# Optimization experiments

Measured on AMD Instinct MI355X. Metric: run time of the kernel, lower is better.

Reference implementation:

```python
import jax, jax.numpy as jnp
import numpy as np


def setup_inputs() -> dict:
    key = jax.random.key(0)
    k1, k2, k3, k4 = jax.random.split(key, 4)
    B, IN_DIM, OUT_DIM = 2048, 4096, 4096
    inputs = jax.random.normal(k1, (B, IN_DIM), dtype=jnp.float32)
    # integer weight code: each element of the implicit (in_dim,out_dim) weight
    # matrix is an index into the per-row `mean` vector of length in_dim
    indices = jax.random.randint(k2, (IN_DIM, OUT_DIM), 0, IN_DIM, dtype=jnp.int32)
    mean = jax.random.normal(k3, (IN_DIM,), dtype=jnp.float32)
    bias = jax.random.normal(k4, (OUT_DIM,), dtype=jnp.float32)
    return {"inputs": inputs, "indices": indices, "mean": mean, "bias": bias}


def reference(inputs, indices, mean, bias):
    # 'unsort' op: decode weight W[i,j] = mean[indices[i,j]], then x @ W
    W = mean[indices]                      # (in_dim, out_dim) gather-decode
    out = jnp.einsum("bi,io->bo", inputs, W)  # (batch, out_dim)
    return out + bias                      # channels_last bias add
```

## Files before the change

kernel.cpp:

```cpp
#include <hip/hip_runtime.h>
#include <hip/hip_bf16.h>


#define M_DIM 2048
#define K_DIM 4096
#define N_DIM 4096

typedef __attribute__((ext_vector_type(8))) short short8v;
typedef __attribute__((ext_vector_type(4))) float f32x4;

__device__ __forceinline__ unsigned short f2bf(float x) {
    unsigned u = __builtin_bit_cast(unsigned, x);
    u += 0x7fffu + ((u >> 16) & 1u);
    return (unsigned short)(u >> 16);
}

__device__ __forceinline__ void gload_lds16(const void* g, void* l) {
    __builtin_amdgcn_global_load_lds(
        (const __attribute__((address_space(1))) void*)(uintptr_t)g,
        (__attribute__((address_space(3))) void*)(uintptr_t)l, 16, 0, 0);
}

__global__ void convert_a_kernel(const float* __restrict__ A,
                                 unsigned short* __restrict__ Abf) {
    int i = blockIdx.x * blockDim.x + threadIdx.x;
    const float4 v = ((const float4*)A)[i];
    ushort4 o;
    o.x = f2bf(v.x); o.y = f2bf(v.y); o.z = f2bf(v.z); o.w = f2bf(v.w);
    ((ushort4*)Abf)[i] = o;
}

__global__ void decode_transpose_kernel(const int* __restrict__ idx,
                                        const float* __restrict__ mean,
                                        unsigned short* __restrict__ Wt) {
    __shared__ float smean[K_DIM];
    __shared__ unsigned short tile[64][65];
    const int t = threadIdx.x;
    for (int i = t; i < K_DIM; i += 256) smean[i] = mean[i];
    __syncthreads();

    const int k0 = blockIdx.y * 64;
    const int n0 = blockIdx.x * 64;
    const int rb = t >> 4;
    const int cb = (t & 15) * 4;

    #pragma unroll
    for (int i = 0; i < 4; ++i) {
        const int r = rb + i * 16;
        const int4 v = *(const int4*)&idx[(size_t)(k0 + r) * N_DIM + n0 + cb];
        tile[cb + 0][r] = f2bf(smean[v.x]);
        tile[cb + 1][r] = f2bf(smean[v.y]);
        tile[cb + 2][r] = f2bf(smean[v.z]);
        tile[cb + 3][r] = f2bf(smean[v.w]);
    }
    __syncthreads();

    #pragma unroll
    for (int i = 0; i < 4; ++i) {
        const int r = rb + i * 16;
        ushort4 o;
        o.x = tile[r][cb + 0];
        o.y = tile[r][cb + 1];
        o.z = tile[r][cb + 2];
        o.w = tile[r][cb + 3];
        *(ushort4*)&Wt[(size_t)(n0 + r) * K_DIM + k0 + cb] = o;
    }
}

__global__ void gemm_kernel(const unsigned short* __restrict__ Abf,
                            const unsigned short* __restrict__ Wt,
                            const float* __restrict__ bias,
                            float* __restrict__ C) {
    __shared__ unsigned short sA[128 * 32];
    __shared__ unsigned short sB[128 * 32];

    const int tid  = threadIdx.x;
    const int lane = tid & 63;
    const int w    = tid >> 6;
    const int wm   = w >> 1, wn = w & 1;
    const int m0   = blockIdx.y * 128;
    const int n0   = blockIdx.x * 128;

    f32x4 acc[4][4] = {};

    const int r0   = tid >> 2;
    const int sub0 = (tid & 3) * 16;

    const int lr = lane & 15;
    const int kq = lane >> 4;

    for (int k0 = 0; k0 < K_DIM; k0 += 32) {
        const char* gA0 = (const char*)(Abf + (size_t)(m0 + r0) * K_DIM + k0) + sub0;
        const char* gA1 = (const char*)(Abf + (size_t)(m0 + 64 + r0) * K_DIM + k0) + sub0;
        const char* gB0 = (const char*)(Wt  + (size_t)(n0 + r0) * K_DIM + k0) + sub0;
        const char* gB1 = (const char*)(Wt  + (size_t)(n0 + 64 + r0) * K_DIM + k0) + sub0;
        gload_lds16(gA0, (char*)sA + tid * 16);
        gload_lds16(gA1, (char*)sA + 4096 + tid * 16);
        gload_lds16(gB0, (char*)sB + tid * 16);
        gload_lds16(gB1, (char*)sB + 4096 + tid * 16);
        __syncthreads();

        short8v a[4], b[4];
        #pragma unroll
        for (int i = 0; i < 4; ++i) {
            a[i] = *(const short8v*)&sA[(wm * 64 + i * 16 + lr) * 32 + kq * 8];
            b[i] = *(const short8v*)&sB[(wn * 64 + i * 16 + lr) * 32 + kq * 8];
        }
        #pragma unroll
        for (int i = 0; i < 4; ++i)
            #pragma unroll
            for (int j = 0; j < 4; ++j)
                acc[i][j] = __builtin_amdgcn_mfma_f32_16x16x32_bf16(a[i], b[j], acc[i][j], 0, 0, 0);
        __syncthreads();
    }

    #pragma unroll
    for (int j = 0; j < 4; ++j) {
        const int n = n0 + wn * 64 + j * 16 + lr;
        const float bv = bias[n];
        #pragma unroll
        for (int i = 0; i < 4; ++i) {
            const int mb = m0 + wm * 64 + i * 16 + kq * 4;
            #pragma unroll
            for (int q = 0; q < 4; ++q)
                C[(size_t)(mb + q) * N_DIM + n] = acc[i][j][q] + bv;
        }
    }
}

extern "C" void kernel_launch(void* const* d_in, const int* in_sizes, int n_in,
                              void* d_out, int out_size, void* d_ws, size_t ws_size,
                              hipStream_t stream) {
    const float* inputs  = (const float*)d_in[0];
    const int*   indices = (const int*)  d_in[1];
    const float* mean    = (const float*)d_in[2];
    const float* bias    = (const float*)d_in[3];
    float* out = (float*)d_out;

    unsigned short* Abf = (unsigned short*)d_ws;
    unsigned short* Wt  = (unsigned short*)((char*)d_ws + (size_t)M_DIM * K_DIM * 2);

    convert_a_kernel<<<(M_DIM * K_DIM / 4) / 256, 256, 0, stream>>>(inputs, Abf);
    decode_transpose_kernel<<<dim3(N_DIM / 64, K_DIM / 64), 256, 0, stream>>>(indices, mean, Wt);
    gemm_kernel<<<dim3(N_DIM / 128, M_DIM / 128), 256, 0, stream>>>(Abf, Wt, bias, out);
}
```

Before: 228.2 us.

## Rewrite GEMM with triple-buffered LDS pipeline, larger tiles and swizzle

```diff
diff --git a/kernel.cpp b/kernel.cpp
--- a/kernel.cpp
+++ b/kernel.cpp
@@ -5,6 +5,14 @@
 #define M_DIM 2048
 #define K_DIM 4096
 #define N_DIM 4096
+
+#define BM 128
+#define BN 256
+#define BK 64
+#define NT (K_DIM / BK)
+#define LDSA_BYTES (BM * BK * 2)
+#define LDSB_BYTES (BN * BK * 2)
+#define LDS_TILE   (LDSA_BYTES + LDSB_BYTES)
 
 typedef __attribute__((ext_vector_type(8))) short short8v;
 typedef __attribute__((ext_vector_type(4))) float f32x4;
@@ -67,52 +75,132 @@
     }
 }
 
-__global__ void gemm_kernel(const unsigned short* __restrict__ Abf,
-                            const unsigned short* __restrict__ Wt,
-                            const float* __restrict__ bias,
-                            float* __restrict__ C) {
-    __shared__ unsigned short sA[128 * 32];
-    __shared__ unsigned short sB[128 * 32];
+
+#define VM6 asm volatile("s_waitcnt vmcnt(6)" ::: "memory")
+#define VM0 asm volatile("s_waitcnt vmcnt(0)" ::: "memory")
+#define NOPST ((void)0)
+
+#define STG_FIRST(kst) do {                          \
+    gload_lds16(srcA0 + (kst), pb2 + ldsA0);         \
+    gload_lds16(srcA1 + (kst), pb2 + ldsA1);         \
+    gload_lds16(srcB0 + (kst), pb2 + ldsB0);         \
+} while (0)
+
+#define STG_SECOND(kst) do {                         \
+    gload_lds16(srcB1 + (kst), pb2 + ldsB1);         \
+    gload_lds16(srcB2 + (kst), pb2 + ldsB2);         \
+    gload_lds16(srcB3 + (kst), pb2 + ldsB3);         \
+} while (0)
+
+#define PHASE(kk, STAGES, ENDW) do {                                          \
+    const int sc = ((((kk) * 4) + kq) ^ (lr & 7)) * 16;                       \
+    short8v a0 = *(const short8v*)(pb0 + rA0 + sc);                           \
+    short8v a1 = *(const short8v*)(pb0 + rA1 + sc);                           \
+    short8v a2 = *(const short8v*)(pb0 + rA2 + sc);                           \
+    short8v a3 = *(const short8v*)(pb0 + rA3 + sc);                           \
+    short8v b0 = *(const short8v*)(pb0 + rB0 + sc);                           \
+    short8v b1 = *(const short8v*)(pb0 + rB1 + sc);                           \
+    short8v b2 = *(const short8v*)(pb0 + rB2 + sc);                           \
+    short8v b3 = *(const short8v*)(pb0 + rB3 + sc);                           \
+    STAGES;                                                                   \
+    __builtin_amdgcn_s_barrier();                                             \
+    __builtin_amdgcn_s_setprio(1);                                            \
+    acc[0][0] = __builtin_amdgcn_mfma_f32_16x16x32_bf16(a0, b0, acc[0][0], 0, 0, 0); \
+    acc[0][1] = __builtin_amdgcn_mfma_f32_16x16x32_bf16(a0, b1, acc[0][1], 0, 0, 0); \
+    acc[0][2] = __builtin_amdgcn_mfma_f32_16x16x32_bf16(a0, b2, acc[0][2], 0, 0, 0); \
+    acc[0][3] = __builtin_amdgcn_mfma_f32_16x16x32_bf16(a0, b3, acc[0][3], 0, 0, 0); \
+    acc[1][0] = __builtin_amdgcn_mfma_f32_16x16x32_bf16(a1, b0, acc[1][0], 0, 0, 0); \
+    acc[1][1] = __builtin_amdgcn_mfma_f32_16x16x32_bf16(a1, b1, acc[1][1], 0, 0, 0); \
+    acc[1][2] = __builtin_amdgcn_mfma_f32_16x16x32_bf16(a1, b2, acc[1][2], 0, 0, 0); \
+    acc[1][3] = __builtin_amdgcn_mfma_f32_16x16x32_bf16(a1, b3, acc[1][3], 0, 0, 0); \
+    acc[2][0] = __builtin_amdgcn_mfma_f32_16x16x32_bf16(a2, b0, acc[2][0], 0, 0, 0); \
+    acc[2][1] = __builtin_amdgcn_mfma_f32_16x16x32_bf16(a2, b1, acc[2][1], 0, 0, 0); \
+    acc[2][2] = __builtin_amdgcn_mfma_f32_16x16x32_bf16(a2, b2, acc[2][2], 0, 0, 0); \
+    acc[2][3] = __builtin_amdgcn_mfma_f32_16x16x32_bf16(a2, b3, acc[2][3], 0, 0, 0); \
+    acc[3][0] = __builtin_amdgcn_mfma_f32_16x16x32_bf16(a3, b0, acc[3][0], 0, 0, 0); \
+    acc[3][1] = __builtin_amdgcn_mfma_f32_16x16x32_bf16(a3, b1, acc[3][1], 0, 0, 0); \
+    acc[3][2] = __builtin_amdgcn_mfma_f32_16x16x32_bf16(a3, b2, acc[3][2], 0, 0, 0); \
+    acc[3][3] = __builtin_amdgcn_mfma_f32_16x16x32_bf16(a3, b3, acc[3][3], 0, 0, 0); \
+    __builtin_amdgcn_s_setprio(0);                                            \
+    ENDW;                                                                     \
+    __builtin_amdgcn_s_barrier();                                             \
+    __builtin_amdgcn_sched_barrier(0);                                        \
+} while (0)
+
+__global__ __launch_bounds__(512, 2) void gemm_kernel(
+        const unsigned short* __restrict__ Abf,
+        const unsigned short* __restrict__ Wt,
+        const float* __restrict__ bias,
+        float* __restrict__ C) {
+    __shared__ __align__(128) char lds[3 * LDS_TILE];
 
     const int tid  = threadIdx.x;
     const int lane = tid & 63;
     const int w    = tid >> 6;
-    const int wm   = w >> 1, wn = w & 1;
-    const int m0   = blockIdx.y * 128;
-    const int n0   = blockIdx.x * 128;
+    const int wm   = w >> 2;
+    const int wn   = w & 3;
+    const int lr   = lane & 15;
+    const int kq   = lane >> 4;
+
+    const int bid = blockIdx.x;
+    const int wg  = (bid & 7) * 32 + (bid >> 3);
+    const int m0  = (wg >> 4) * BM;
+    const int n0  = (wg & 15) * BN;
+
+    const int pA0 = tid,        pA1 = 512 + tid;
+    const int pB0 = tid,        pB1 = 512 + tid;
+    const int pB2 = 1024 + tid, pB3 = 1536 + tid;
+    const unsigned short* srcA0 = Abf + (size_t)(m0 + (pA0 >> 3)) * K_DIM + 8 * ((pA0 & 7) ^ ((pA0 >> 3) & 7));
+    const unsigned short* srcA1 = Abf + (size_t)(m0 + (pA1 >> 3)) * K_DIM + 8 * ((pA1 & 7) ^ ((pA1 >> 3) & 7));
+    const unsigned short* srcB0 = Wt  + (size_t)(n0 + (pB0 >> 3)) * K_DIM + 8 * ((pB0 & 7) ^ ((pB0 >> 3) & 7));
+    const unsigned short* srcB1 = Wt  + (size_t)(n0 + (pB1 >> 3)) * K_DIM + 8 * ((pB1 & 7) ^ ((pB1 >> 3) & 7));
+    const unsigned short* srcB2 = Wt  + (size_t)(n0 + (pB2 >> 3)) * K_DIM + 8 * ((pB2 & 7) ^ ((pB2 >> 3) & 7));
+    const unsigned short* srcB3 = Wt  + (size_t)(n0 + (pB3 >> 3)) * K_DIM + 8 * ((pB3 & 7) ^ ((pB3 >> 3) & 7));
+    const int ldsA0 = pA0 * 16, ldsA1 = pA1 * 16;
+    const int ldsB0 = LDSA_BYTES + pB0 * 16, ldsB1 = LDSA_BYTES + pB1 * 16;
+    const int ldsB2 = LDSA_BYTES + pB2 * 16, ldsB3 = LDSA_BYTES + pB3 * 16;
+
+    const int rA0 = (wm * 64 +  0 + lr) * 128;
+    const int rA1 = (wm * 64 + 16 + lr) * 128;
+    const int rA2 = (wm * 64 + 32 + lr) * 128;
+    const int rA3 = (wm * 64 + 48 + lr) * 128;
+    const int rB0 = LDSA_BYTES + (wn * 64 +  0 + lr) * 128;
+    const int rB1 = LDSA_BYTES + (wn * 64 + 16 + lr) * 128;
+    const int rB2 = LDSA_BYTES + (wn * 64 + 32 + lr) * 128;
+    const int rB3 = LDSA_BYTES + (wn * 64 + 48 + lr) * 128;
+
+    char* pb0 = (char*)lds;
+    char* pb1 = (char*)lds + LDS_TILE;
+    char* pb2 = (char*)lds + 2 * LDS_TILE;
 
     f32x4 acc[4][4] = {};
 
-    const int r0   = tid >> 2;
-    const int sub0 = (tid & 3) * 16;
-
-    const int lr = lane & 15;
-    const int kq = lane >> 4;
-
-    for (int k0 = 0; k0 < K_DIM; k0 += 32) {
-        const char* gA0 = (const char*)(Abf + (size_t)(m0 + r0) * K_DIM + k0) + sub0;
-        const char* gA1 = (const char*)(Abf + (size_t)(m0 + 64 + r0) * K_DIM + k0) + sub0;
-        const char* gB0 = (const char*)(Wt  + (size_t)(n0 + r0) * K_DIM + k0) + sub0;
-        const char* gB1 = (const char*)(Wt  + (size_t)(n0 + 64 + r0) * K_DIM + k0) + sub0;
-        gload_lds16(gA0, (char*)sA + tid * 16);
-        gload_lds16(gA1, (char*)sA + 4096 + tid * 16);
-        gload_lds16(gB0, (char*)sB + tid * 16);
-        gload_lds16(gB1, (char*)sB + 4096 + tid * 16);
-        __syncthreads();
-
-        short8v a[4], b[4];
-        #pragma unroll
-        for (int i = 0; i < 4; ++i) {
-            a[i] = *(const short8v*)&sA[(wm * 64 + i * 16 + lr) * 32 + kq * 8];
-            b[i] = *(const short8v*)&sB[(wn * 64 + i * 16 + lr) * 32 + kq * 8];
-        }
-        #pragma unroll
-        for (int i = 0; i < 4; ++i)
-            #pragma unroll
-            for (int j = 0; j < 4; ++j)
-                acc[i][j] = __builtin_amdgcn_mfma_f32_16x16x32_bf16(a[i], b[j], acc[i][j], 0, 0, 0);
-        __syncthreads();
-    }
+    gload_lds16(srcA0 + 0, pb0 + ldsA0);
+    gload_lds16(srcA1 + 0, pb0 + ldsA1);
+    gload_lds16(srcB0 + 0, pb0 + ldsB0);
+    gload_lds16(srcB1 + 0, pb0 + ldsB1);
+    gload_lds16(srcB2 + 0, pb0 + ldsB2);
+    gload_lds16(srcB3 + 0, pb0 + ldsB3);
+    gload_lds16(srcA0 + BK, pb1 + ldsA0);
+    gload_lds16(srcA1 + BK, pb1 + ldsA1);
+    gload_lds16(srcB0 + BK, pb1 + ldsB0);
+    gload_lds16(srcB1 + BK, pb1 + ldsB1);
+    gload_lds16(srcB2 + BK, pb1 + ldsB2);
+    gload_lds16(srcB3 + BK, pb1 + ldsB3);
+    VM6;
+    __builtin_amdgcn_s_barrier();
+
+    for (int t = 0; t < NT - 2; ++t) {
+        const int kst = (t + 2) * BK;
+        PHASE(0, STG_FIRST(kst), NOPST);
+        PHASE(1, STG_SECOND(kst), VM6);
+        char* tmp = pb0; pb0 = pb1; pb1 = pb2; pb2 = tmp;
+    }
+    PHASE(0, NOPST, NOPST);
+    PHASE(1, NOPST, VM0);
+    pb0 = pb1;
+    PHASE(0, NOPST, NOPST);
+    PHASE(1, NOPST, NOPST);
 
     #pragma unroll
     for (int j = 0; j < 4; ++j) {
@@ -142,5 +230,5 @@
 
     convert_a_kernel<<<(M_DIM * K_DIM / 4) / 256, 256, 0, stream>>>(inputs, Abf);
     decode_transpose_kernel<<<dim3(N_DIM / 64, K_DIM / 64), 256, 0, stream>>>(indices, mean, Wt);
-    gemm_kernel<<<dim3(N_DIM / 128, M_DIM / 128), 256, 0, stream>>>(Abf, Wt, bias, out);
-}
+    gemm_kernel<<<256, 512, 0, stream>>>(Abf, Wt, bias, out);
+}
```

Result: faster. 209.8 us (-8.1%).

## Rewrite GEMM with 4-stage LDS pipeline, 128x256 tiles, swizzle and XCD remap

Applied to the files above, without the earlier changes.

```diff
diff --git a/kernel.cpp b/kernel.cpp
--- a/kernel.cpp
+++ b/kernel.cpp
@@ -5,6 +5,14 @@
 #define M_DIM 2048
 #define K_DIM 4096
 #define N_DIM 4096
+
+#define BM 128
+#define BN 256
+#define BK 32
+#define NT (K_DIM / BK)
+#define TILE_A (BM * BK * 2)
+#define TILE_B (BN * BK * 2)
+#define TILE   (TILE_A + TILE_B)
 
 typedef __attribute__((ext_vector_type(8))) short short8v;
 typedef __attribute__((ext_vector_type(4))) float f32x4;
@@ -67,60 +75,150 @@
     }
 }
 
-__global__ void gemm_kernel(const unsigned short* __restrict__ Abf,
-                            const unsigned short* __restrict__ Wt,
-                            const float* __restrict__ bias,
-                            float* __restrict__ C) {
-    __shared__ unsigned short sA[128 * 32];
-    __shared__ unsigned short sB[128 * 32];
+
+#define VM6  asm volatile("s_waitcnt vmcnt(6)" ::: "memory")
+#define VM0  asm volatile("s_waitcnt vmcnt(0)" ::: "memory")
+#define VM12 asm volatile("s_waitcnt vmcnt(12)" ::: "memory")
+
+#define STAGE(buf, t) do {                          \
+    const int ko_ = (t) * BK;                       \
+    gload_lds16(sA0 + ko_, (buf) + lA0);            \
+    gload_lds16(sA1 + ko_, (buf) + lA1);            \
+    gload_lds16(sB0 + ko_, (buf) + lB0);            \
+    gload_lds16(sB1 + ko_, (buf) + lB1);            \
+    gload_lds16(sB2 + ko_, (buf) + lB2);            \
+    gload_lds16(sB3 + ko_, (buf) + lB3);            \
+} while (0)
+
+#define READ(aS, bS, buf) do {                      \
+    aS[0] = *(const short8v*)((buf) + rA0);         \
+    aS[1] = *(const short8v*)((buf) + rA1);         \
+    aS[2] = *(const short8v*)((buf) + rA2);         \
+    aS[3] = *(const short8v*)((buf) + rA3);         \
+    aS[4] = *(const short8v*)((buf) + rA4);         \
+    aS[5] = *(const short8v*)((buf) + rA5);         \
+    aS[6] = *(const short8v*)((buf) + rA6);         \
+    aS[7] = *(const short8v*)((buf) + rA7);         \
+    bS[0] = *(const short8v*)((buf) + rB0);         \
+    bS[1] = *(const short8v*)((buf) + rB1);         \
+    bS[2] = *(const short8v*)((buf) + rB2);         \
+    bS[3] = *(const short8v*)((buf) + rB3);         \
+} while (0)
+
+#define MM1(aS, bS, i, j) \
+    acc[i][j] = __builtin_amdgcn_mfma_f32_16x16x32_bf16(aS[i], bS[j], acc[i][j], 0, 0, 0)
+
+#define MM(aS, bS) do {                                              \
+    MM1(aS,bS,0,0); MM1(aS,bS,0,1); MM1(aS,bS,0,2); MM1(aS,bS,0,3);  \
+    MM1(aS,bS,1,0); MM1(aS,bS,1,1); MM1(aS,bS,1,2); MM1(aS,bS,1,3);  \
+    MM1(aS,bS,2,0); MM1(aS,bS,2,1); MM1(aS,bS,2,2); MM1(aS,bS,2,3);  \
+    MM1(aS,bS,3,0); MM1(aS,bS,3,1); MM1(aS,bS,3,2); MM1(aS,bS,3,3);  \
+    MM1(aS,bS,4,0); MM1(aS,bS,4,1); MM1(aS,bS,4,2); MM1(aS,bS,4,3);  \
+    MM1(aS,bS,5,0); MM1(aS,bS,5,1); MM1(aS,bS,5,2); MM1(aS,bS,5,3);  \
+    MM1(aS,bS,6,0); MM1(aS,bS,6,1); MM1(aS,bS,6,2); MM1(aS,bS,6,3);  \
+    MM1(aS,bS,7,0); MM1(aS,bS,7,1); MM1(aS,bS,7,2); MM1(aS,bS,7,3);  \
+} while (0)
+
+#define ITER_FULL(t, cA, cB, nA, nB, rdbuf, stbuf) do {  \
+    VM6;                                                 \
+    __builtin_amdgcn_s_barrier();                        \
+    READ(nA, nB, rdbuf);                                 \
+    STAGE(stbuf, (t) + 3);                               \
+    __builtin_amdgcn_sched_barrier(0);                   \
+    __builtin_amdgcn_s_setprio(1);                       \
+    MM(cA, cB);                                          \
+    __builtin_amdgcn_s_setprio(0);                       \
+} while (0)
+
+__global__ __launch_bounds__(256, 1) void gemm_kernel(
+        const unsigned short* __restrict__ Abf,
+        const unsigned short* __restrict__ Wt,
+        const float* __restrict__ bias,
+        float* __restrict__ C) {
+    __shared__ __align__(128) char lds[4 * TILE];
 
     const int tid  = threadIdx.x;
     const int lane = tid & 63;
-    const int w    = tid >> 6;
-    const int wm   = w >> 1, wn = w & 1;
-    const int m0   = blockIdx.y * 128;
-    const int n0   = blockIdx.x * 128;
-
-    f32x4 acc[4][4] = {};
-
-    const int r0   = tid >> 2;
-    const int sub0 = (tid & 3) * 16;
-
-    const int lr = lane & 15;
-    const int kq = lane >> 4;
-
-    for (int k0 = 0; k0 < K_DIM; k0 += 32) {
-        const char* gA0 = (const char*)(Abf + (size_t)(m0 + r0) * K_DIM + k0) + sub0;
-        const char* gA1 = (const char*)(Abf + (size_t)(m0 + 64 + r0) * K_DIM + k0) + sub0;
-        const char* gB0 = (const char*)(Wt  + (size_t)(n0 + r0) * K_DIM + k0) + sub0;
-        const char* gB1 = (const char*)(Wt  + (size_t)(n0 + 64 + r0) * K_DIM + k0) + sub0;
-        gload_lds16(gA0, (char*)sA + tid * 16);
-        gload_lds16(gA1, (char*)sA + 4096 + tid * 16);
-        gload_lds16(gB0, (char*)sB + tid * 16);
-        gload_lds16(gB1, (char*)sB + 4096 + tid * 16);
-        __syncthreads();
-
-        short8v a[4], b[4];
-        #pragma unroll
-        for (int i = 0; i < 4; ++i) {
-            a[i] = *(const short8v*)&sA[(wm * 64 + i * 16 + lr) * 32 + kq * 8];
-            b[i] = *(const short8v*)&sB[(wn * 64 + i * 16 + lr) * 32 + kq * 8];
-        }
-        #pragma unroll
-        for (int i = 0; i < 4; ++i)
-            #pragma unroll
-            for (int j = 0; j < 4; ++j)
-                acc[i][j] = __builtin_amdgcn_mfma_f32_16x16x32_bf16(a[i], b[j], acc[i][j], 0, 0, 0);
-        __syncthreads();
-    }
+    const int wn   = tid >> 6;
+    const int lr   = lane & 15;
+    const int kq   = lane >> 4;
+
+    const int bid = blockIdx.x;
+    const int wg  = (bid & 7) * 32 + (bid >> 3);
+    const int m0  = (wg >> 4) * BM;
+    const int n0  = (wg & 15) * BN;
+
+    const int pA0 = tid,        pA1 = 256 + tid;
+    const int pB0 = tid,        pB1 = 256 + tid;
+    const int pB2 = 512 + tid,  pB3 = 768 + tid;
+#define SRCA(p) (Abf + (size_t)(m0 + ((p) >> 2)) * K_DIM + 8 * ((((p) & 3) - (((p) >> 3) & 3)) & 3))
+#define SRCB(p) (Wt  + (size_t)(n0 + ((p) >> 2)) * K_DIM + 8 * ((((p) & 3) - (((p) >> 3) & 3)) & 3))
+    const unsigned short* sA0 = SRCA(pA0);
+    const unsigned short* sA1 = SRCA(pA1);
+    const unsigned short* sB0 = SRCB(pB0);
+    const unsigned short* sB1 = SRCB(pB1);
+    const unsigned short* sB2 = SRCB(pB2);
+    const unsigned short* sB3 = SRCB(pB3);
+    const int lA0 = pA0 * 16,          lA1 = pA1 * 16;
+    const int lB0 = TILE_A + pB0 * 16, lB1 = TILE_A + pB1 * 16;
+    const int lB2 = TILE_A + pB2 * 16, lB3 = TILE_A + pB3 * 16;
+
+    const int sc  = ((kq + (lr >> 1)) & 3) * 16;
+    const int rA0 = ( 0 * 16 + lr) * 64 + sc;
+    const int rA1 = ( 1 * 16 + lr) * 64 + sc;
+    const int rA2 = ( 2 * 16 + lr) * 64 + sc;
+    const int rA3 = ( 3 * 16 + lr) * 64 + sc;
+    const int rA4 = ( 4 * 16 + lr) * 64 + sc;
+    const int rA5 = ( 5 * 16 + lr) * 64 + sc;
+    const int rA6 = ( 6 * 16 + lr) * 64 + sc;
+    const int rA7 = ( 7 * 16 + lr) * 64 + sc;
+    const int rB0 = TILE_A + (wn * 64 +  0 + lr) * 64 + sc;
+    const int rB1 = TILE_A + (wn * 64 + 16 + lr) * 64 + sc;
+    const int rB2 = TILE_A + (wn * 64 + 32 + lr) * 64 + sc;
+    const int rB3 = TILE_A + (wn * 64 + 48 + lr) * 64 + sc;
+
+    char* b0v = (char*)lds;
+    char* b1v = (char*)lds + TILE;
+    char* b2v = (char*)lds + 2 * TILE;
+    char* b3v = (char*)lds + 3 * TILE;
+
+    f32x4 acc[8][4] = {};
+    short8v aE[8], bE[4], aO[8], bO[4];
+
+    STAGE(b0v, 0);
+    STAGE(b1v, 1);
+    STAGE(b2v, 2);
+    VM12;
+    __builtin_amdgcn_s_barrier();
+    READ(aE, bE, b0v);
+
+    for (int tt = 0; tt < 31; ++tt) {
+        const int t = tt * 4;
+        ITER_FULL(t + 0, aE, bE, aO, bO, b1v, b3v);
+        ITER_FULL(t + 1, aO, bO, aE, bE, b2v, b0v);
+        ITER_FULL(t + 2, aE, bE, aO, bO, b3v, b1v);
+        ITER_FULL(t + 3, aO, bO, aE, bE, b0v, b2v);
+    }
+    ITER_FULL(124, aE, bE, aO, bO, b1v, b3v);
+    VM6;
+    __builtin_amdgcn_s_barrier();
+    READ(aE, bE, b2v);
+    __builtin_amdgcn_sched_barrier(0);
+    MM(aO, bO);
+    VM0;
+    __builtin_amdgcn_s_barrier();
+    READ(aO, bO, b3v);
+    __builtin_amdgcn_sched_barrier(0);
+    MM(aE, bE);
+    MM(aO, bO);
 
     #pragma unroll
     for (int j = 0; j < 4; ++j) {
         const int n = n0 + wn * 64 + j * 16 + lr;
         const float bv = bias[n];
         #pragma unroll
-        for (int i = 0; i < 4; ++i) {
-            const int mb = m0 + wm * 64 + i * 16 + kq * 4;
+        for (int i = 0; i < 8; ++i) {
+            const int mb = m0 + i * 16 + kq * 4;
             #pragma unroll
             for (int q = 0; q < 4; ++q)
                 C[(size_t)(mb + q) * N_DIM + n] = acc[i][j][q] + bv;
@@ -142,5 +240,5 @@
 
     convert_a_kernel<<<(M_DIM * K_DIM / 4) / 256, 256, 0, stream>>>(inputs, Abf);
     decode_transpose_kernel<<<dim3(N_DIM / 64, K_DIM / 64), 256, 0, stream>>>(indices, mean, Wt);
-    gemm_kernel<<<dim3(N_DIM / 128, M_DIM / 128), 256, 0, stream>>>(Abf, Wt, bias, out);
-}
+    gemm_kernel<<<256, 256, 0, stream>>>(Abf, Wt, bias, out);
+}
```

After: 218.5 us. 4.2% less time.

## Rewrite GEMM with triple-buffered LDS pipeline, swizzled layout, larger tiles

Applied to the files above, without the earlier changes.

```diff
diff --git a/kernel.cpp b/kernel.cpp
--- a/kernel.cpp
+++ b/kernel.cpp
@@ -5,6 +5,14 @@
 #define M_DIM 2048
 #define K_DIM 4096
 #define N_DIM 4096
+
+#define BM 128
+#define BN 256
+#define BK 64
+#define NT (K_DIM / BK)
+#define LDSA_BYTES (BM * BK * 2)
+#define LDSB_BYTES (BN * BK * 2)
+#define LDS_TILE   (LDSA_BYTES + LDSB_BYTES)
 
 typedef __attribute__((ext_vector_type(8))) short short8v;
 typedef __attribute__((ext_vector_type(4))) float f32x4;
@@ -67,51 +75,137 @@
     }
 }
 
-__global__ void gemm_kernel(const unsigned short* __restrict__ Abf,
-                            const unsigned short* __restrict__ Wt,
-                            const float* __restrict__ bias,
-                            float* __restrict__ C) {
-    __shared__ unsigned short sA[128 * 32];
-    __shared__ unsigned short sB[128 * 32];
+
+#define VM6  asm volatile("s_waitcnt vmcnt(6)" ::: "memory")
+#define VM0  asm volatile("s_waitcnt vmcnt(0)" ::: "memory")
+
+#define STG6(buf, t) do {                           \
+    const int ko_ = (t) * BK;                       \
+    gload_lds16(sA0 + ko_, (buf) + lA0);            \
+    gload_lds16(sA1 + ko_, (buf) + lA1);            \
+    gload_lds16(sB0 + ko_, (buf) + lB0);            \
+    gload_lds16(sB1 + ko_, (buf) + lB1);            \
+    gload_lds16(sB2 + ko_, (buf) + lB2);            \
+    gload_lds16(sB3 + ko_, (buf) + lB3);            \
+} while (0)
+
+#define READ8(aS, bS, buf, so) do {                 \
+    aS[0] = *(const short8v*)((buf) + rA0 + (so));  \
+    aS[1] = *(const short8v*)((buf) + rA1 + (so));  \
+    aS[2] = *(const short8v*)((buf) + rA2 + (so));  \
+    aS[3] = *(const short8v*)((buf) + rA3 + (so));  \
+    bS[0] = *(const short8v*)((buf) + rB0 + (so));  \
+    bS[1] = *(const short8v*)((buf) + rB1 + (so));  \
+    bS[2] = *(const short8v*)((buf) + rB2 + (so));  \
+    bS[3] = *(const short8v*)((buf) + rB3 + (so));  \
+} while (0)
+
+#define MM1(aS, bS, i, j) \
+    acc[i][j] = __builtin_amdgcn_mfma_f32_16x16x32_bf16(aS[i], bS[j], acc[i][j], 0, 0, 0)
+
+#define MM16(aS, bS) do {                                            \
+    MM1(aS,bS,0,0); MM1(aS,bS,0,1); MM1(aS,bS,0,2); MM1(aS,bS,0,3);  \
+    MM1(aS,bS,1,0); MM1(aS,bS,1,1); MM1(aS,bS,1,2); MM1(aS,bS,1,3);  \
+    MM1(aS,bS,2,0); MM1(aS,bS,2,1); MM1(aS,bS,2,2); MM1(aS,bS,2,3);  \
+    MM1(aS,bS,3,0); MM1(aS,bS,3,1); MM1(aS,bS,3,2); MM1(aS,bS,3,3);  \
+} while (0)
+
+#define ITER(cbuf, sbuf, tstage) do {               \
+    READ8(aE, bE, cbuf, 0);                         \
+    READ8(aO, bO, cbuf, so1);                       \
+    STG6(sbuf, tstage);                             \
+    __builtin_amdgcn_s_setprio(1);                  \
+    MM16(aE, bE);                                   \
+    MM16(aO, bO);                                   \
+    __builtin_amdgcn_s_setprio(0);                  \
+    VM6;                                            \
+    __builtin_amdgcn_s_barrier();                   \
+} while (0)
+
+#define ITER_NOSTG(cbuf, WAITC) do {                \
+    READ8(aE, bE, cbuf, 0);                         \
+    READ8(aO, bO, cbuf, so1);                       \
+    __builtin_amdgcn_s_setprio(1);                  \
+    MM16(aE, bE);                                   \
+    MM16(aO, bO);                                   \
+    __builtin_amdgcn_s_setprio(0);                  \
+    WAITC;                                          \
+    __builtin_amdgcn_s_barrier();                   \
+} while (0)
+
+__global__ __launch_bounds__(512, 2) void gemm_kernel(
+        const unsigned short* __restrict__ Abf,
+        const unsigned short* __restrict__ Wt,
+        const float* __restrict__ bias,
+        float* __restrict__ C) {
+    __shared__ __align__(128) char lds[3 * LDS_TILE];
 
     const int tid  = threadIdx.x;
     const int lane = tid & 63;
     const int w    = tid >> 6;
-    const int wm   = w >> 1, wn = w & 1;
-    const int m0   = blockIdx.y * 128;
-    const int n0   = blockIdx.x * 128;
+    const int wm   = w >> 2;
+    const int wn   = w & 3;
+    const int lr   = lane & 15;
+    const int kq   = lane >> 4;
+
+    const int bid = blockIdx.x;
+    const int wg  = (bid & 7) * 32 + (bid >> 3);
+    const int m0  = (wg >> 4) * BM;
+    const int n0  = (wg & 15) * BN;
+
+    const int pA0 = tid,        pA1 = 512 + tid;
+    const int pB0 = tid,        pB1 = 512 + tid;
+    const int pB2 = 1024 + tid, pB3 = 1536 + tid;
+    const unsigned short* sA0 = Abf + (size_t)(m0 + (pA0 >> 3)) * K_DIM + 8 * ((pA0 & 7) ^ ((pA0 >> 3) & 7));
+    const unsigned short* sA1 = Abf + (size_t)(m0 + (pA1 >> 3)) * K_DIM + 8 * ((pA1 & 7) ^ ((pA1 >> 3) & 7));
+    const unsigned short* sB0 = Wt  + (size_t)(n0 + (pB0 >> 3)) * K_DIM + 8 * ((pB0 & 7) ^ ((pB0 >> 3) & 7));
+    const unsigned short* sB1 = Wt  + (size_t)(n0 + (pB1 >> 3)) * K_DIM + 8 * ((pB1 & 7) ^ ((pB1 >> 3) & 7));
+    const unsigned short* sB2 = Wt  + (size_t)(n0 + (pB2 >> 3)) * K_DIM + 8 * ((pB2 & 7) ^ ((pB2 >> 3) & 7));
+    const unsigned short* sB3 = Wt  + (size_t)(n0 + (pB3 >> 3)) * K_DIM + 8 * ((pB3 & 7) ^ ((pB3 >> 3) & 7));
+    const int lA0 = pA0 * 16,              lA1 = pA1 * 16;
+    const int lB0 = LDSA_BYTES + pB0 * 16, lB1 = LDSA_BYTES + pB1 * 16;
+    const int lB2 = LDSA_BYTES + pB2 * 16, lB3 = LDSA_BYTES + pB3 * 16;
+
+    const int c0  = kq ^ (lr & 7);
+    const int sc  = c0 * 16;
+    const int so1 = ((c0 ^ 4) - c0) * 16;
+    const int rA0 = (wm * 64 +  0 + lr) * 128 + sc;
+    const int rA1 = (wm * 64 + 16 + lr) * 128 + sc;
+    const int rA2 = (wm * 64 + 32 + lr) * 128 + sc;
+    const int rA3 = (wm * 64 + 48 + lr) * 128 + sc;
+    const int rB0 = LDSA_BYTES + (wn * 64 +  0 + lr) * 128 + sc;
+    const int rB1 = LDSA_BYTES + (wn * 64 + 16 + lr) * 128 + sc;
+    const int rB2 = LDSA_BYTES + (wn * 64 + 32 + lr) * 128 + sc;
+    const int rB3 = LDSA_BYTES + (wn * 64 + 48 + lr) * 128 + sc;
+
+    char* b0v = (char*)lds;
+    char* b1v = (char*)lds + LDS_TILE;
+    char* b2v = (char*)lds + 2 * LDS_TILE;
 
     f32x4 acc[4][4] = {};
-
-    const int r0   = tid >> 2;
-    const int sub0 = (tid & 3) * 16;
-
-    const int lr = lane & 15;
-    const int kq = lane >> 4;
-
-    for (int k0 = 0; k0 < K_DIM; k0 += 32) {
-        const char* gA0 = (const char*)(Abf + (size_t)(m0 + r0) * K_DIM + k0) + sub0;
-        const char* gA1 = (const char*)(Abf + (size_t)(m0 + 64 + r0) * K_DIM + k0) + sub0;
-        const char* gB0 = (const char*)(Wt  + (size_t)(n0 + r0) * K_DIM + k0) + sub0;
-        const char* gB1 = (const char*)(Wt  + (size_t)(n0 + 64 + r0) * K_DIM + k0) + sub0;
-        gload_lds16(gA0, (char*)sA + tid * 16);
-        gload_lds16(gA1, (char*)sA + 4096 + tid * 16);
-        gload_lds16(gB0, (char*)sB + tid * 16);
-        gload_lds16(gB1, (char*)sB + 4096 + tid * 16);
-        __syncthreads();
-
-        short8v a[4], b[4];
-        #pragma unroll
-        for (int i = 0; i < 4; ++i) {
-            a[i] = *(const short8v*)&sA[(wm * 64 + i * 16 + lr) * 32 + kq * 8];
-            b[i] = *(const short8v*)&sB[(wn * 64 + i * 16 + lr) * 32 + kq * 8];
-        }
-        #pragma unroll
-        for (int i = 0; i < 4; ++i)
-            #pragma unroll
-            for (int j = 0; j < 4; ++j)
-                acc[i][j] = __builtin_amdgcn_mfma_f32_16x16x32_bf16(a[i], b[j], acc[i][j], 0, 0, 0);
-        __syncthreads();
+    short8v aE[4], bE[4], aO[4], bO[4];
+
+    STG6(b0v, 0);
+    STG6(b1v, 1);
+    VM6;
+    __builtin_amdgcn_s_barrier();
+
+    for (int tt = 0; tt < 20; ++tt) {
+        const int t = tt * 3;
+        ITER(b0v, b2v, t + 2);
+        ITER(b1v, b0v, t + 3);
+        ITER(b2v, b1v, t + 4);
+    }
+    ITER(b0v, b2v, 62);
+    ITER(b1v, b0v, 63);
+    ITER_NOSTG(b2v, VM0);
+    {
+        READ8(aE, bE, b0v, 0);
+        READ8(aO, bO, b0v, so1);
+        __builtin_amdgcn_s_setprio(1);
+        MM16(aE, bE);
+        MM16(aO, bO);
+        __builtin_amdgcn_s_setprio(0);
     }
 
     #pragma unroll
@@ -142,5 +236,5 @@
 
     convert_a_kernel<<<(M_DIM * K_DIM / 4) / 256, 256, 0, stream>>>(inputs, Abf);
     decode_transpose_kernel<<<dim3(N_DIM / 64, K_DIM / 64), 256, 0, stream>>>(indices, mean, Wt);
-    gemm_kernel<<<dim3(N_DIM / 128, M_DIM / 128), 256, 0, stream>>>(Abf, Wt, bias, out);
-}
+    gemm_kernel<<<256, 512, 0, stream>>>(Abf, Wt, bias, out);
+}
```

Measured after the change: 203.1 us. 11.0% less time.
